# Optimization experiments

Hardware: AMD Instinct MI355X
Metric: run time of the kernel (lower is better)

Reference implementation:

```python
import jax, jax.numpy as jnp
import numpy as np

E = 1024   # embed_dim
H = 16     # num_heads
D = E // H # head dim = 64
NUM_BUCKETS = 32
MAX_DISTANCE = 128


def _relative_position_bucket(rel, num_buckets=NUM_BUCKETS, max_distance=MAX_DISTANCE):
    # T5-style bucketing (bidirectional): sign half + log-spaced far buckets.
    nb = num_buckets // 2
    buckets = (rel > 0).astype(jnp.int32) * nb
    rel = jnp.abs(rel)
    max_exact = nb // 2
    is_small = rel < max_exact
    # clamp to >=1 before log to avoid -inf on the masked-out branch
    rel_f = jnp.maximum(rel, 1).astype(jnp.float32)
    large = max_exact + (
        jnp.log(rel_f / max_exact) / np.log(max_distance / max_exact) * (nb - max_exact)
    ).astype(jnp.int32)
    large = jnp.minimum(large, nb - 1)
    return buckets + jnp.where(is_small, rel, large)


def setup_inputs() -> dict:
    key = jax.random.key(0)
    ks = jax.random.split(key, 6)
    B, S, K = 2, 2048, 2048
    w = 0.02
    return {
        "hidden_states": jax.random.normal(ks[0], (B, S, E), jnp.float32),
        "key_value_states": jax.random.normal(ks[1], (B, K, E), jnp.float32),
        "Wq": jax.random.normal(ks[2], (E, E), jnp.float32) * w,
        "Wkv": jax.random.normal(ks[3], (E, 2 * E), jnp.float32) * w,
        "Wo": jax.random.normal(ks[4], (E, E), jnp.float32) * w,
        "rel_bias": jax.random.normal(ks[5], (NUM_BUCKETS, H), jnp.float32) * w,
    }


def reference(hidden_states, key_value_states, Wq, Wkv, Wo, rel_bias):
    B, S, _ = hidden_states.shape
    K = key_value_states.shape[1]
    # projections (no bias, no 1/sqrt(d) scaling — T5 style)
    q = (hidden_states @ Wq).reshape(B, S, H, D).transpose(0, 2, 1, 3)      # [B,H,S,D]
    kv = (key_value_states @ Wkv).reshape(B, K, 2, H, D)
    k = kv[:, :, 0].transpose(0, 2, 1, 3)                                   # [B,H,K,D]
    v = kv[:, :, 1].transpose(0, 2, 1, 3)                                   # [B,H,K,D]
    scores = jnp.einsum('bhsd,bhkd->bhsk', q, k)                            # [B,H,S,K]
    # relative position bias
    rel = jnp.arange(K)[None, :] - jnp.arange(S)[:, None]                   # [S,K]
    buckets = _relative_position_bucket(rel)                                # [S,K]
    bias = rel_bias[buckets].transpose(2, 0, 1)[None]                       # [1,H,S,K]
    scores = scores + bias
    attn = jax.nn.softmax(scores.astype(jnp.float32), axis=-1).astype(scores.dtype)
    out = jnp.einsum('bhsk,bhkd->bshd', attn, v).reshape(B, S, E)
    return out @ Wo
```

## Files before the change

### kernel.cpp

```cpp
#include <hip/hip_runtime.h>
#include <hip/hip_bf16.h>
#include <math.h>

typedef __hip_bfloat16 bf16;
typedef __bf16 bf16x4 __attribute__((ext_vector_type(4)));
typedef __bf16 bf16x8 __attribute__((ext_vector_type(8)));
typedef float f32x4 __attribute__((ext_vector_type(4)));
typedef float f32x16 __attribute__((ext_vector_type(16)));
typedef unsigned short us4 __attribute__((ext_vector_type(4)));

#define LOG2E 1.44269504088896340736f

#if defined(__has_builtin)
#if __has_builtin(__builtin_amdgcn_exp2f)
#define EXP2(x) __builtin_amdgcn_exp2f(x)
#else
#define EXP2(x) exp2f(x)
#endif
#else
#define EXP2(x) exp2f(x)
#endif

__device__ inline __bf16 f2b(float f) {
  __hip_bfloat16 h = __float2bfloat16(f);
  return *reinterpret_cast<__bf16*>(&h);
}
__device__ inline unsigned short b2u(float f) {
  __hip_bfloat16 h = __float2bfloat16(f);
  return *reinterpret_cast<unsigned short*>(&h);
}
__device__ inline unsigned short b2u_fast(float f) {
  union { float f; unsigned u; } v;
  v.f = f;
  return (unsigned short)((v.u + 0x8000u) >> 16);
}
__device__ inline bf16x8 ld16(const bf16* p) {
  bf16x4 lo = *(const bf16x4*)p;
  bf16x4 hi = *(const bf16x4*)(p + 4);
  return __builtin_shufflevector(lo, hi, 0, 1, 2, 3, 4, 5, 6, 7);
}
__device__ inline void st16(bf16* p, uint4 v) {
  *(uint2*)p = make_uint2(v.x, v.y);
  *(uint2*)(p + 4) = make_uint2(v.z, v.w);
}
__device__ inline void async16(const bf16* g, bf16* l) {
  __builtin_amdgcn_global_load_lds(
      (const __attribute__((address_space(1))) unsigned int*)g,
      (__attribute__((address_space(3))) unsigned int*)l, 16, 0, 0);
}

__global__ void cast_k(const float* __restrict__ in, bf16* __restrict__ out, int n) {
  int i = (blockIdx.x * 256 + threadIdx.x) * 8;
  if (i >= n) return;
  float4 a0 = *(const float4*)(in + i);
  float4 a1 = *(const float4*)(in + i + 4);
  bf16x8 v;
  v[0] = f2b(a0.x); v[1] = f2b(a0.y); v[2] = f2b(a0.z); v[3] = f2b(a0.w);
  v[4] = f2b(a1.x); v[5] = f2b(a1.y); v[6] = f2b(a1.z); v[7] = f2b(a1.w);
  *(bf16x8*)(out + i) = v;
}

__global__ void transpose_cast_k(const float* __restrict__ in, bf16* __restrict__ out,
                                 int rows, int cols) {
  __shared__ float tile[32][33];
  int c0 = blockIdx.x * 32;
  int r0 = blockIdx.y * 32;
  int tx = threadIdx.x;
  int ty = threadIdx.y;
  for (int i = ty; i < 32; i += 8)
    tile[i][tx] = in[(size_t)(r0 + i) * cols + c0 + tx];
  __syncthreads();
  for (int i = ty; i < 32; i += 8)
    out[(size_t)(c0 + i) * rows + r0 + tx] = __float2bfloat16(tile[tx][i]);
}

__global__ void bias_lut_k(const float* __restrict__ rel_bias, float* __restrict__ lut) {
  int r = blockIdx.x * blockDim.x + threadIdx.x;
  if (r >= 4096) return;
  int rel = r - 2048;
  int b = rel > 0 ? 16 : 0;
  int ar = rel < 0 ? -rel : rel;
  int idx;
  if (ar < 8) {
    idx = b + ar;
  } else {
    double t = log((double)ar / 8.0) / log(16.0) * 8.0;
    int lg = 8 + (int)t;
    if (lg > 15) lg = 15;
    idx = b + lg;
  }
  for (int h = 0; h < 16; ++h)
    lut[h * 4096 + r] = rel_bias[idx * 16 + h] * LOG2E;
}

__global__ __launch_bounds__(256) void gemm_qkv_k(const bf16* __restrict__ hbf,
                                                  const bf16* __restrict__ kbf,
                                                  const bf16* __restrict__ WqT,
                                                  const bf16* __restrict__ WkvT,
                                                  bf16* __restrict__ Qb,
                                                  bf16* __restrict__ Kb,
                                                  bf16* __restrict__ Vt) {
  __shared__ __align__(16) bf16 As[128 * 32];
  __shared__ __align__(16) bf16 Bs[128 * 32];
  const int tid = threadIdx.x;
  const int lane = tid & 63;
  const int w = tid >> 6;
  const int wm = (w >> 1) * 64;
  const int wn = (w & 1) * 64;
  const int l15 = lane & 15;
  const int quad = lane >> 4;
  const int srow = lane >> 2;
  const int skg = lane & 3;

  const bool isQ = blockIdx.y < 8;
  const bf16* A = isQ ? hbf : kbf;
  const bf16* Bt = isQ ? WqT : WkvT;
  const int n0 = (isQ ? blockIdx.y : blockIdx.y - 8) * 128;
  const int m0 = blockIdx.x * 128;

  f32x4 acc[4][4];
#pragma unroll
  for (int i = 0; i < 4; ++i)
#pragma unroll
    for (int j = 0; j < 4; ++j) acc[i][j] = (f32x4){0.f, 0.f, 0.f, 0.f};

  for (int k0 = 0; k0 < 1024; k0 += 32) {
    __syncthreads();
#pragma unroll
    for (int rep = 0; rep < 2; ++rep) {
      int seg = w * 2 + rep;
      async16(A + (size_t)(m0 + seg * 16 + srow) * 1024 + k0 + skg * 8, As + seg * 512);
      async16(Bt + (size_t)(n0 + seg * 16 + srow) * 1024 + k0 + skg * 8, Bs + seg * 512);
    }
    __syncthreads();
    bf16x8 af[4], bfr[4];
#pragma unroll
    for (int i = 0; i < 4; ++i)
      af[i] = *(const bf16x8*)(As + (wm + i * 16 + l15) * 32 + quad * 8);
#pragma unroll
    for (int j = 0; j < 4; ++j)
      bfr[j] = *(const bf16x8*)(Bs + (wn + j * 16 + l15) * 32 + quad * 8);
#pragma unroll
    for (int i = 0; i < 4; ++i)
#pragma unroll
      for (int j = 0; j < 4; ++j)
        acc[i][j] = __builtin_amdgcn_mfma_f32_16x16x32_bf16(af[i], bfr[j], acc[i][j], 0, 0, 0);
  }

  if (!isQ && n0 >= 1024) {
#pragma unroll
    for (int i = 0; i < 4; ++i) {
      int gmb = m0 + wm + i * 16 + quad * 4;
      int b = gmb >> 11, kp = gmb & 2047;
#pragma unroll
      for (int j = 0; j < 4; ++j) {
        int gn = n0 + wn + j * 16 + l15;
        int h = (gn >> 6) & 15, d = gn & 63;
        us4 pk;
#pragma unroll
        for (int r = 0; r < 4; ++r) pk[r] = b2u(acc[i][j][r]);
        *(us4*)(Vt + ((((size_t)b * 16 + h) * 64 + d) << 11) + kp) = pk;
      }
    }
    return;
  }
  const float scale = isQ ? LOG2E : 1.0f;
#pragma unroll
  for (int i = 0; i < 4; ++i)
#pragma unroll
    for (int j = 0; j < 4; ++j)
#pragma unroll
      for (int r = 0; r < 4; ++r) {
        int gm = m0 + wm + i * 16 + quad * 4 + r;
        int gn = n0 + wn + j * 16 + l15;
        bf16 v = __float2bfloat16(acc[i][j][r] * scale);
        int b = gm >> 11, s = gm & 2047;
        int h = (gn >> 6) & 15, d = gn & 63;
        bf16* dst = isQ ? Qb : Kb;
        dst[((((size_t)b * 16 + h) * 2048 + s) << 6) + d] = v;
      }
}

__global__ __launch_bounds__(256) void gemm_o_k(const bf16* __restrict__ A,
                                                const bf16* __restrict__ Bt,
                                                float* __restrict__ C0) {
  __shared__ __align__(16) bf16 As[128 * 32];
  __shared__ __align__(16) bf16 Bs[64 * 32];
  const int tid = threadIdx.x;
  const int lane = tid & 63;
  const int w = tid >> 6;
  const int wm = w * 32;
  const int m0 = blockIdx.x * 128;
  const int n0 = blockIdx.y * 64;
  const int l15 = lane & 15;
  const int quad = lane >> 4;
  const int srow = lane >> 2;
  const int skg = lane & 3;

  f32x4 acc[2][4];
#pragma unroll
  for (int i = 0; i < 2; ++i)
#pragma unroll
    for (int j = 0; j < 4; ++j) acc[i][j] = (f32x4){0.f, 0.f, 0.f, 0.f};

  for (int k0 = 0; k0 < 1024; k0 += 32) {
    __syncthreads();
#pragma unroll
    for (int rep = 0; rep < 2; ++rep) {
      int seg = w * 2 + rep;
      async16(A + (size_t)(m0 + seg * 16 + srow) * 1024 + k0 + skg * 8, As + seg * 512);
    }
    async16(Bt + (size_t)(n0 + w * 16 + srow) * 1024 + k0 + skg * 8, Bs + w * 512);
    __syncthreads();
    bf16x8 af[2], bfr[4];
#pragma unroll
    for (int i = 0; i < 2; ++i)
      af[i] = *(const bf16x8*)(As + (wm + i * 16 + l15) * 32 + quad * 8);
#pragma unroll
    for (int j = 0; j < 4; ++j)
      bfr[j] = *(const bf16x8*)(Bs + (j * 16 + l15) * 32 + quad * 8);
#pragma unroll
    for (int i = 0; i < 2; ++i)
#pragma unroll
      for (int j = 0; j < 4; ++j)
        acc[i][j] = __builtin_amdgcn_mfma_f32_16x16x32_bf16(af[i], bfr[j], acc[i][j], 0, 0, 0);
  }
#pragma unroll
  for (int i = 0; i < 2; ++i)
#pragma unroll
    for (int j = 0; j < 4; ++j)
#pragma unroll
      for (int r = 0; r < 4; ++r) {
        int gm = m0 + wm + i * 16 + quad * 4 + r;
        int gn = n0 + j * 16 + l15;
        C0[(size_t)gm * 1024 + gn] = acc[i][j][r];
      }
}

#define STK 68
#define SVK 136
__global__ __launch_bounds__(256) void attn_k(const bf16* __restrict__ Qb,
                                              const bf16* __restrict__ Kb,
                                              const bf16* __restrict__ Vt,
                                              const float* __restrict__ lut,
                                              bf16* __restrict__ Ob) {
  __shared__ float lbias[2176];
  __shared__ __align__(16) bf16 Ks[128 * STK];
  __shared__ __align__(16) bf16 Vs[64 * SVK];
  __shared__ __align__(16) bf16 Ps[128 * SVK];

  const int tid = threadIdx.x;
  const int lane = tid & 63;
  const int w = tid >> 6;
  const int q31 = lane & 31;
  const int half = lane >> 5;

  const int qt = blockIdx.x;
  const int bh = blockIdx.y;
  const int h = bh & 15, b = bh >> 4;
  const int qb = qt * 128;

  const int gbase = h * 4096 + 1921 - qb;
  for (int t = tid; t < 2175; t += 256) lbias[t] = lut[gbase + t];

  const size_t base = (size_t)bh * 2048 * 64;
  const size_t vbase = (size_t)bh * 64 * 2048;
  const int qg = qb + w * 32 + q31;

  bf16x8 qf[4];
#pragma unroll
  for (int c = 0; c < 4; ++c)
    qf[c] = *(const bf16x8*)(Qb + base + (size_t)qg * 64 + c * 16 + half * 8);

  f32x16 oacc[2];
#pragma unroll
  for (int dj = 0; dj < 2; ++dj)
#pragma unroll
    for (int r = 0; r < 16; ++r) oacc[dj][r] = 0.f;
  float m_run = -INFINITY, l_run = 0.f;

  bf16* prow = Ps + (w * 32 + q31) * SVK;

  for (int kt = 0; kt < 2048; kt += 128) {
    __syncthreads();
#pragma unroll
    for (int rep = 0; rep < 4; ++rep) {
      int slot = tid + rep * 256;
      int kk = slot >> 3, cg = slot & 7;
      uint4 kv = *(const uint4*)(Kb + base + (size_t)(kt + kk) * 64 + cg * 8);
      st16(Ks + kk * STK + cg * 8, kv);
      int d = slot >> 4, c = slot & 15;
      uint4 vv = *(const uint4*)(Vt + vbase + (size_t)d * 2048 + kt + c * 8);
      st16(Vs + d * SVK + c * 8, vv);
    }
    __syncthreads();

    f32x16 sacc[4];
#pragma unroll
    for (int mt = 0; mt < 4; ++mt) {
#pragma unroll
      for (int r = 0; r < 16; ++r) sacc[mt][r] = 0.f;
#pragma unroll
      for (int c = 0; c < 4; ++c) {
        bf16x8 kf = ld16(Ks + (mt * 32 + q31) * STK + c * 16 + half * 8);
        sacc[mt] = __builtin_amdgcn_mfma_f32_32x32x16_bf16(kf, qf[c], sacc[mt], 0, 0, 0);
      }
    }

    const int xbase = kt + 127 + 4 * half - w * 32 - q31;
    float mx = -INFINITY;
#pragma unroll
    for (int mt = 0; mt < 4; ++mt)
#pragma unroll
      for (int g = 0; g < 4; ++g) {
        int x0 = xbase + mt * 32 + 8 * g;
#pragma unroll
        for (int rr = 0; rr < 4; ++rr) {
          float s = sacc[mt][4 * g + rr] + lbias[x0 + rr];
          sacc[mt][4 * g + rr] = s;
          mx = fmaxf(mx, s);
        }
      }
    mx = fmaxf(mx, __shfl_xor(mx, 32));
    float mnew = fmaxf(m_run, mx);
    float alpha = EXP2(m_run - mnew);
    m_run = mnew;
    float sum = 0.f;
#pragma unroll
    for (int mt = 0; mt < 4; ++mt)
#pragma unroll
      for (int r = 0; r < 16; ++r) {
        float p = EXP2(sacc[mt][r] - mnew);
        sacc[mt][r] = p;
        sum += p;
      }
    sum += __shfl_xor(sum, 32);
    l_run = l_run * alpha + sum;

#pragma unroll
    for (int mt = 0; mt < 4; ++mt)
#pragma unroll
      for (int g = 0; g < 4; ++g) {
        us4 pk;
#pragma unroll
        for (int rr = 0; rr < 4; ++rr) pk[rr] = b2u_fast(sacc[mt][4 * g + rr]);
        *(us4*)(prow + mt * 32 + 8 * g + 4 * half) = pk;
      }

#pragma unroll
    for (int dj = 0; dj < 2; ++dj)
#pragma unroll
      for (int r = 0; r < 16; ++r) oacc[dj][r] *= alpha;

    bf16x8 pf[8];
#pragma unroll
    for (int c = 0; c < 8; ++c) pf[c] = ld16(prow + c * 16 + half * 8);
#pragma unroll
    for (int dj = 0; dj < 2; ++dj)
#pragma unroll
      for (int c = 0; c < 8; ++c) {
        bf16x8 vf = ld16(Vs + (dj * 32 + q31) * SVK + c * 16 + half * 8);
        oacc[dj] = __builtin_amdgcn_mfma_f32_32x32x16_bf16(vf, pf[c], oacc[dj], 0, 0, 0);
      }
  }

  float inv = 1.0f / l_run;
#pragma unroll
  for (int dj = 0; dj < 2; ++dj)
#pragma unroll
    for (int g = 0; g < 4; ++g) {
      us4 pk;
#pragma unroll
      for (int rr = 0; rr < 4; ++rr) pk[rr] = b2u(oacc[dj][4 * g + rr] * inv);
      int d0 = dj * 32 + 8 * g + 4 * half;
      *(us4*)(Ob + ((size_t)(b * 2048 + qg)) * 1024 + h * 64 + d0) = pk;
    }
}

extern "C" void kernel_launch(void* const* d_in, const int* in_sizes, int n_in,
                              void* d_out, int out_size, void* d_ws, size_t ws_size,
                              hipStream_t stream) {
  const float* hidden = (const float*)d_in[0];
  const float* kvs    = (const float*)d_in[1];
  const float* Wq     = (const float*)d_in[2];
  const float* Wkv    = (const float*)d_in[3];
  const float* Wo     = (const float*)d_in[4];
  const float* relb   = (const float*)d_in[5];
  float* out = (float*)d_out;

  char* ws = (char*)d_ws;
  bf16* WqT  = (bf16*)(ws + (size_t)0);
  bf16* WkvT = (bf16*)(ws + ((size_t)2 << 20));
  bf16* WoT  = (bf16*)(ws + ((size_t)6 << 20));
  bf16* Ob   = (bf16*)(ws + ((size_t)8 << 20));
  bf16* hbf  = Ob;
  bf16* Qb   = (bf16*)(ws + ((size_t)16 << 20));
  bf16* Kb   = (bf16*)(ws + ((size_t)24 << 20));
  bf16* Vt   = (bf16*)(ws + ((size_t)32 << 20));
  float* LUT = (float*)(ws + ((size_t)40 << 20));
  bf16* kbf  = (bf16*)d_out;

  dim3 tb(32, 8);
  transpose_cast_k<<<dim3(32, 32), tb, 0, stream>>>(Wq, WqT, 1024, 1024);
  transpose_cast_k<<<dim3(64, 32), tb, 0, stream>>>(Wkv, WkvT, 1024, 2048);
  transpose_cast_k<<<dim3(32, 32), tb, 0, stream>>>(Wo, WoT, 1024, 1024);
  bias_lut_k<<<16, 256, 0, stream>>>(relb, LUT);
  cast_k<<<2048, 256, 0, stream>>>(hidden, hbf, 4194304);
  cast_k<<<2048, 256, 0, stream>>>(kvs, kbf, 4194304);

  gemm_qkv_k<<<dim3(32, 24), 256, 0, stream>>>(hbf, kbf, WqT, WkvT, Qb, Kb, Vt);
  attn_k<<<dim3(16, 32), 256, 0, stream>>>(Qb, Kb, Vt, LUT, Ob);
  gemm_o_k<<<dim3(32, 16), 256, 0, stream>>>(Ob, WoT, out);
}
```

Baseline: 253.0 us.

## Prefetch K/V tiles into registers, keep P in registers, vectorize GEMM epilogues

The attention kernel now loads the next K/V tile into registers while the current tile is computed, which hides global load latency behind the MFMA work. It also drops the Ps shared-memory round trip by exchanging the bf16 P fragments across lane halves with shuffles. The Q/K and O GEMMs swap their MFMA operands so each lane holds contiguous columns, which allows vector stores in the epilogue. The weight transposes are merged into one launch and the two input casts into another, cutting launch count. The register prefetch and shuffles raise register pressure, which can lower occupancy.

```diff
diff --git a/kernel.cpp b/kernel.cpp
--- a/kernel.cpp
+++ b/kernel.cpp
@@ -43,15 +43,29 @@
   *(uint2*)p = make_uint2(v.x, v.y);
   *(uint2*)(p + 4) = make_uint2(v.z, v.w);
 }
+__device__ inline us4 shfl32_us4(us4 v) {
+  uint2 u = *(uint2*)&v;
+  u.x = __shfl_xor(u.x, 32);
+  u.y = __shfl_xor(u.y, 32);
+  return *(us4*)&u;
+}
+__device__ inline bf16x8 mk8(us4 lo, us4 hi) {
+  bf16x4 l = *(bf16x4*)&lo;
+  bf16x4 h = *(bf16x4*)&hi;
+  return __builtin_shufflevector(l, h, 0, 1, 2, 3, 4, 5, 6, 7);
+}
 __device__ inline void async16(const bf16* g, bf16* l) {
   __builtin_amdgcn_global_load_lds(
       (const __attribute__((address_space(1))) unsigned int*)g,
       (__attribute__((address_space(3))) unsigned int*)l, 16, 0, 0);
 }
 
-__global__ void cast_k(const float* __restrict__ in, bf16* __restrict__ out, int n) {
-  int i = (blockIdx.x * 256 + threadIdx.x) * 8;
-  if (i >= n) return;
+__global__ void cast2_k(const float* __restrict__ a, const float* __restrict__ b,
+                        bf16* __restrict__ oa, bf16* __restrict__ ob) {
+  int gid = blockIdx.x * 256 + threadIdx.x;
+  const float* in = (gid < 524288) ? a : b;
+  bf16* out = (gid < 524288) ? oa : ob;
+  int i = (gid & 524287) * 8;
   float4 a0 = *(const float4*)(in + i);
   float4 a1 = *(const float4*)(in + i + 4);
   bf16x8 v;
@@ -60,18 +74,23 @@
   *(bf16x8*)(out + i) = v;
 }
 
-__global__ void transpose_cast_k(const float* __restrict__ in, bf16* __restrict__ out,
-                                 int rows, int cols) {
+__global__ void transpose_all_k(const float* __restrict__ Wq, const float* __restrict__ Wkv,
+                                const float* __restrict__ Wo, bf16* __restrict__ WqT,
+                                bf16* __restrict__ WkvT, bf16* __restrict__ WoT) {
   __shared__ float tile[32][33];
+  int z = blockIdx.z;
+  const float* in = z == 0 ? Wq : (z == 1 ? Wkv : Wo);
+  bf16* out = z == 0 ? WqT : (z == 1 ? WkvT : WoT);
+  int cols = z == 1 ? 2048 : 1024;
   int c0 = blockIdx.x * 32;
+  if (c0 >= cols) return;
   int r0 = blockIdx.y * 32;
-  int tx = threadIdx.x;
-  int ty = threadIdx.y;
+  int tx = threadIdx.x, ty = threadIdx.y;
   for (int i = ty; i < 32; i += 8)
     tile[i][tx] = in[(size_t)(r0 + i) * cols + c0 + tx];
   __syncthreads();
   for (int i = ty; i < 32; i += 8)
-    out[(size_t)(c0 + i) * rows + r0 + tx] = __float2bfloat16(tile[tx][i]);
+    out[(size_t)(c0 + i) * 1024 + r0 + tx] = __float2bfloat16(tile[tx][i]);
 }
 
 __global__ void bias_lut_k(const float* __restrict__ rel_bias, float* __restrict__ lut) {
@@ -117,6 +136,7 @@
   const bf16* Bt = isQ ? WqT : WkvT;
   const int n0 = (isQ ? blockIdx.y : blockIdx.y - 8) * 128;
   const int m0 = blockIdx.x * 128;
+  const bool isV = (!isQ) && (n0 >= 1024);
 
   f32x4 acc[4][4];
 #pragma unroll
@@ -140,14 +160,22 @@
 #pragma unroll
     for (int j = 0; j < 4; ++j)
       bfr[j] = *(const bf16x8*)(Bs + (wn + j * 16 + l15) * 32 + quad * 8);
-#pragma unroll
-    for (int i = 0; i < 4; ++i)
-#pragma unroll
-      for (int j = 0; j < 4; ++j)
-        acc[i][j] = __builtin_amdgcn_mfma_f32_16x16x32_bf16(af[i], bfr[j], acc[i][j], 0, 0, 0);
-  }
-
-  if (!isQ && n0 >= 1024) {
+    if (isV) {
+#pragma unroll
+      for (int i = 0; i < 4; ++i)
+#pragma unroll
+        for (int j = 0; j < 4; ++j)
+          acc[i][j] = __builtin_amdgcn_mfma_f32_16x16x32_bf16(af[i], bfr[j], acc[i][j], 0, 0, 0);
+    } else {
+#pragma unroll
+      for (int i = 0; i < 4; ++i)
+#pragma unroll
+        for (int j = 0; j < 4; ++j)
+          acc[i][j] = __builtin_amdgcn_mfma_f32_16x16x32_bf16(bfr[j], af[i], acc[i][j], 0, 0, 0);
+    }
+  }
+
+  if (isV) {
 #pragma unroll
     for (int i = 0; i < 4; ++i) {
       int gmb = m0 + wm + i * 16 + quad * 4;
@@ -165,20 +193,21 @@
     return;
   }
   const float scale = isQ ? LOG2E : 1.0f;
-#pragma unroll
-  for (int i = 0; i < 4; ++i)
-#pragma unroll
-    for (int j = 0; j < 4; ++j)
-#pragma unroll
-      for (int r = 0; r < 4; ++r) {
-        int gm = m0 + wm + i * 16 + quad * 4 + r;
-        int gn = n0 + wn + j * 16 + l15;
-        bf16 v = __float2bfloat16(acc[i][j][r] * scale);
-        int b = gm >> 11, s = gm & 2047;
-        int h = (gn >> 6) & 15, d = gn & 63;
-        bf16* dst = isQ ? Qb : Kb;
-        dst[((((size_t)b * 16 + h) * 2048 + s) << 6) + d] = v;
-      }
+  bf16* dst = isQ ? Qb : Kb;
+#pragma unroll
+  for (int i = 0; i < 4; ++i) {
+    int gm = m0 + wm + i * 16 + l15;
+    int b = gm >> 11, s = gm & 2047;
+#pragma unroll
+    for (int j = 0; j < 4; ++j) {
+      int gn = n0 + wn + j * 16 + quad * 4;
+      int h = (gn >> 6) & 15, d0 = gn & 63;
+      us4 pk;
+#pragma unroll
+      for (int r = 0; r < 4; ++r) pk[r] = b2u(acc[i][j][r] * scale);
+      *(us4*)(dst + ((((size_t)b * 16 + h) * 2048 + s) << 6) + d0) = pk;
+    }
+  }
 }
 
 __global__ __launch_bounds__(256) void gemm_o_k(const bf16* __restrict__ A,
@@ -223,18 +252,17 @@
     for (int i = 0; i < 2; ++i)
 #pragma unroll
       for (int j = 0; j < 4; ++j)
-        acc[i][j] = __builtin_amdgcn_mfma_f32_16x16x32_bf16(af[i], bfr[j], acc[i][j], 0, 0, 0);
-  }
-#pragma unroll
-  for (int i = 0; i < 2; ++i)
-#pragma unroll
-    for (int j = 0; j < 4; ++j)
-#pragma unroll
-      for (int r = 0; r < 4; ++r) {
-        int gm = m0 + wm + i * 16 + quad * 4 + r;
-        int gn = n0 + j * 16 + l15;
-        C0[(size_t)gm * 1024 + gn] = acc[i][j][r];
-      }
+        acc[i][j] = __builtin_amdgcn_mfma_f32_16x16x32_bf16(bfr[j], af[i], acc[i][j], 0, 0, 0);
+  }
+#pragma unroll
+  for (int i = 0; i < 2; ++i) {
+    int gm = m0 + wm + i * 16 + l15;
+#pragma unroll
+    for (int j = 0; j < 4; ++j) {
+      int gn = n0 + j * 16 + quad * 4;
+      *(f32x4*)(C0 + (size_t)gm * 1024 + gn) = acc[i][j];
+    }
+  }
 }
 
 #define STK 68
@@ -247,7 +275,6 @@
   __shared__ float lbias[2176];
   __shared__ __align__(16) bf16 Ks[128 * STK];
   __shared__ __align__(16) bf16 Vs[64 * SVK];
-  __shared__ __align__(16) bf16 Ps[128 * SVK];
 
   const int tid = threadIdx.x;
   const int lane = tid & 63;
@@ -279,21 +306,31 @@
     for (int r = 0; r < 16; ++r) oacc[dj][r] = 0.f;
   float m_run = -INFINITY, l_run = 0.f;
 
-  bf16* prow = Ps + (w * 32 + q31) * SVK;
+  uint4 kreg[4], vreg[4];
+#pragma unroll
+  for (int rep = 0; rep < 4; ++rep) {
+    int slot = tid + rep * 256;
+    kreg[rep] = *(const uint4*)(Kb + base + (size_t)(slot >> 3) * 64 + (slot & 7) * 8);
+    vreg[rep] = *(const uint4*)(Vt + vbase + (size_t)(slot >> 4) * 2048 + (slot & 15) * 8);
+  }
 
   for (int kt = 0; kt < 2048; kt += 128) {
     __syncthreads();
 #pragma unroll
     for (int rep = 0; rep < 4; ++rep) {
       int slot = tid + rep * 256;
-      int kk = slot >> 3, cg = slot & 7;
-      uint4 kv = *(const uint4*)(Kb + base + (size_t)(kt + kk) * 64 + cg * 8);
-      st16(Ks + kk * STK + cg * 8, kv);
-      int d = slot >> 4, c = slot & 15;
-      uint4 vv = *(const uint4*)(Vt + vbase + (size_t)d * 2048 + kt + c * 8);
-      st16(Vs + d * SVK + c * 8, vv);
-    }
-    __syncthreads();
+      st16(Ks + (slot >> 3) * STK + (slot & 7) * 8, kreg[rep]);
+      st16(Vs + (slot >> 4) * SVK + (slot & 15) * 8, vreg[rep]);
+    }
+    __syncthreads();
+    if (kt + 128 < 2048) {
+#pragma unroll
+      for (int rep = 0; rep < 4; ++rep) {
+        int slot = tid + rep * 256;
+        kreg[rep] = *(const uint4*)(Kb + base + (size_t)(kt + 128 + (slot >> 3)) * 64 + (slot & 7) * 8);
+        vreg[rep] = *(const uint4*)(Vt + vbase + (size_t)(slot >> 4) * 2048 + kt + 128 + (slot & 15) * 8);
+      }
+    }
 
     f32x16 sacc[4];
 #pragma unroll
@@ -337,31 +374,38 @@
     sum += __shfl_xor(sum, 32);
     l_run = l_run * alpha + sum;
 
-#pragma unroll
-    for (int mt = 0; mt < 4; ++mt)
-#pragma unroll
-      for (int g = 0; g < 4; ++g) {
+    us4 ownq[4][4], rcv[4][2];
+#pragma unroll
+    for (int mt = 0; mt < 4; ++mt) {
+#pragma unroll
+      for (int a = 0; a < 4; ++a) {
         us4 pk;
 #pragma unroll
-        for (int rr = 0; rr < 4; ++rr) pk[rr] = b2u_fast(sacc[mt][4 * g + rr]);
-        *(us4*)(prow + mt * 32 + 8 * g + 4 * half) = pk;
-      }
+        for (int bb = 0; bb < 4; ++bb) pk[bb] = b2u_fast(sacc[mt][4 * a + bb]);
+        ownq[mt][a] = pk;
+      }
+      us4 s0 = half ? ownq[mt][0] : ownq[mt][1];
+      us4 s1 = half ? ownq[mt][2] : ownq[mt][3];
+      rcv[mt][0] = shfl32_us4(s0);
+      rcv[mt][1] = shfl32_us4(s1);
+    }
 
 #pragma unroll
     for (int dj = 0; dj < 2; ++dj)
 #pragma unroll
       for (int r = 0; r < 16; ++r) oacc[dj][r] *= alpha;
 
-    bf16x8 pf[8];
-#pragma unroll
-    for (int c = 0; c < 8; ++c) pf[c] = ld16(prow + c * 16 + half * 8);
-#pragma unroll
-    for (int dj = 0; dj < 2; ++dj)
-#pragma unroll
-      for (int c = 0; c < 8; ++c) {
+#pragma unroll
+    for (int c = 0; c < 8; ++c) {
+      int mt = c >> 1, p = c & 1;
+      bf16x8 pfc = half ? mk8(rcv[mt][p], ownq[mt][2 * p + 1])
+                        : mk8(ownq[mt][2 * p], rcv[mt][p]);
+#pragma unroll
+      for (int dj = 0; dj < 2; ++dj) {
         bf16x8 vf = ld16(Vs + (dj * 32 + q31) * SVK + c * 16 + half * 8);
-        oacc[dj] = __builtin_amdgcn_mfma_f32_32x32x16_bf16(vf, pf[c], oacc[dj], 0, 0, 0);
-      }
+        oacc[dj] = __builtin_amdgcn_mfma_f32_32x32x16_bf16(vf, pfc, oacc[dj], 0, 0, 0);
+      }
+    }
   }
 
   float inv = 1.0f / l_run;
@@ -400,13 +444,9 @@
   float* LUT = (float*)(ws + ((size_t)40 << 20));
   bf16* kbf  = (bf16*)d_out;
 
-  dim3 tb(32, 8);
-  transpose_cast_k<<<dim3(32, 32), tb, 0, stream>>>(Wq, WqT, 1024, 1024);
-  transpose_cast_k<<<dim3(64, 32), tb, 0, stream>>>(Wkv, WkvT, 1024, 2048);
-  transpose_cast_k<<<dim3(32, 32), tb, 0, stream>>>(Wo, WoT, 1024, 1024);
+  transpose_all_k<<<dim3(64, 32, 3), dim3(32, 8), 0, stream>>>(Wq, Wkv, Wo, WqT, WkvT, WoT);
   bias_lut_k<<<16, 256, 0, stream>>>(relb, LUT);
-  cast_k<<<2048, 256, 0, stream>>>(hidden, hbf, 4194304);
-  cast_k<<<2048, 256, 0, stream>>>(kvs, kbf, 4194304);
+  cast2_k<<<4096, 256, 0, stream>>>(hidden, kvs, hbf, kbf);
 
   gemm_qkv_k<<<dim3(32, 24), 256, 0, stream>>>(hbf, kbf, WqT, WkvT, Qb, Kb, Vt);
   attn_k<<<dim3(16, 32), 256, 0, stream>>>(Qb, Kb, Vt, LUT, Ob);
```

Result: faster. 233.9 us (-7.5%).
